# Kernel optimization log

Hardware: AMD Instinct MI355X
Metric: run time of the kernel (lower is better)

Reference implementation:

```python
import jax, jax.numpy as jnp
import numpy as np
from jax import lax

B, C, H, W = 16, 8, 512, 512
HW = H * W
AX = int(np.floor(0.1 * HW))  # torch: int(np.floor(0.1 * H * W))
EPS = 1e-5


def roberts_kernels():
    # Two 2x2 Roberts cross kernels, OIHW layout [2,1,2,2]
    kx = np.array([[1.0, 0.0], [0.0, -1.0]], np.float32)
    ky = np.array([[0.0, 1.0], [-1.0, 0.0]], np.float32)
    return jnp.asarray(np.stack([kx, ky])[:, None])


def edge_maps(x, kernels):
    # x: [N,1,H,W] -> gradient magnitude flattened to [N, HW]
    g = lax.conv_general_dilated(
        x, kernels, window_strides=(1, 1), padding=[(0, 1), (0, 1)],
        dimension_numbers=("NCHW", "OIHW", "NCHW"))  # [N,2,H,W]
    mag = jnp.sqrt(g[:, 0] ** 2 + g[:, 1] ** 2 + 1e-12)
    return mag.reshape(x.shape[0], -1)


def setup_inputs() -> dict:
    key = jax.random.key(0)
    k1, k2 = jax.random.split(key)
    return {
        "predictions": jax.random.normal(k1, (B, C, H, W), jnp.float32),
        "target": jax.random.normal(k2, (B, C, H, W), jnp.float32),
        "alpha": jnp.ones((), jnp.float32),
        "kernels": roberts_kernels(),
    }


def _forward(predictions, target, alpha, kernels):
    N = B * C
    et_all = edge_maps(target.reshape(N, 1, H, W), kernels)       # [N,HW]
    ep_all = edge_maps(predictions.reshape(N, 1, H, W), kernels)  # [N,HW]

    # Faithful to the original: edge_T_final/edge_P_final persist across
    # the (i,j) loop, so the scatter state is carried sequentially.
    def step(carry, xs):
        etf, epf = carry
        et_i, ep_i = xs
        _, tb = lax.top_k(et_i, AX)
        etf = etf.at[tb].set(et_i[tb])
        _, pb = lax.top_k(ep_i, AX)
        epf = epf.at[pb].set(ep_i[pb])
        row = jnp.abs((etf - epf) / (etf + epf + EPS))
        return (etf, epf), row

    init = (jnp.zeros(HW, jnp.float32), jnp.zeros(HW, jnp.float32))
    _, edge = lax.scan(step, init, (et_all, ep_all))  # edge: [N,HW]
    return alpha * jnp.mean(edge)


def reference(predictions, target, alpha, kernels):
    return _forward(predictions, target, alpha, kernels)
```

## Files before the change

### kernel.cpp

```cpp
#include <hip/hip_runtime.h>
#include <stdint.h>

#define H 512
#define W 512
#define HW (H * W)
#define NIMG 128
#define AX 26214
#define NB 8192
#define CAND_CAP 7168

__device__ __forceinline__ float4 f4zero() { return make_float4(0.f, 0.f, 0.f, 0.f); }

__device__ __forceinline__ void block_select(uint32_t* hist, uint32_t* chunkSuf,
                                             uint32_t* outBin, uint32_t* outRank,
                                             uint32_t K) {
  int tid = threadIdx.x;
  if (tid < 512) {
    int base = tid * 16;
    uint32_t csum = 0;
#pragma unroll
    for (int k = 0; k < 16; k++) csum += hist[base + k];
    chunkSuf[tid] = csum;
  }
  __syncthreads();
  if (tid < 64) {
    uint32_t cs[8];
    uint32_t g = 0;
#pragma unroll
    for (int m = 0; m < 8; m++) { cs[m] = chunkSuf[tid * 8 + m]; g += cs[m]; }
    uint32_t v = g;
#pragma unroll
    for (int off = 1; off < 64; off <<= 1) {
      uint32_t u = __shfl_down(v, off);
      if (tid + off < 64) v += u;
    }
    uint32_t run = v - g;
    for (int m = 7; m >= 0; m--) {
      chunkSuf[tid * 8 + m] = run;
      run += cs[m];
    }
  }
  __syncthreads();
  if (tid < 512) {
    int base = tid * 16;
    uint32_t run = chunkSuf[tid];
    for (int k = 15; k >= 0; k--) {
      uint32_t h = hist[base + k];
      if (run < K && run + h >= K) {
        *outBin = (uint32_t)(base + k);
        *outRank = K - run;
      }
      run += h;
    }
  }
  __syncthreads();
}

template <int PASS>
__device__ __forceinline__ void select_pass(const float* __restrict__ x,
                                            uint32_t* hist, uint32_t* cand,
                                            uint32_t* sCnt, uint32_t b0) {
  int tid = threadIdx.x;
  int wl = tid & 63;
  int lane_c = (tid & 127) << 2;
  int r0 = (tid >> 7) << 6;
  const bool haveE = lane_c + 4 < W;

  float4 vA, vB, vC, vD;
  float eA = 0.f, eB = 0.f, eC = 0.f, eD = 0.f;
#define LDROW(r, v, e)                                        \
  {                                                           \
    if ((r) < H) {                                            \
      v = *(const float4*)(x + (r) * W + lane_c);             \
      if (wl == 63) e = haveE ? x[(r) * W + lane_c + 4] : 0.f;\
    } else { v = f4zero(); e = 0.f; }                         \
  }
  LDROW(r0, vA, eA)
  LDROW(r0 + 1, vB, eB)
  LDROW(r0 + 2, vC, eC)
  for (int it = 0; it < 64; ++it) {
    int r = r0 + it;
    if (it < 62) { LDROW(r + 3, vD, eD) } else { vD = f4zero(); eD = 0.f; }
    float ea = __shfl(vA.x, wl + 1); if (wl == 63) ea = eA;
    float eb = __shfl(vB.x, wl + 1); if (wl == 63) eb = eB;
    float a[5] = {vA.x, vA.y, vA.z, vA.w, ea};
    float bb[5] = {vB.x, vB.y, vB.z, vB.w, eb};
#pragma unroll
    for (int j = 0; j < 4; j++) {
      float g0 = a[j] - bb[j + 1];
      float g1 = a[j + 1] - bb[j];
      float msq = fmaf(g0, g0, fmaf(g1, g1, 1e-12f));
      uint32_t bits = __float_as_uint(msq);
      if (PASS == 0) {
        atomicAdd(&hist[bits >> 19], 1u);
      } else {
        if ((bits >> 19) == b0) {
          uint32_t idx = atomicAdd(sCnt, 1u);
          if (idx < CAND_CAP) cand[idx] = bits;
        }
      }
    }
    vA = vB; eA = eB; vB = vC; eB = eC; vC = vD; eC = eD;
  }
#undef LDROW
}

__global__ __launch_bounds__(1024) void selectKernel(const float* __restrict__ target,
                                                     const float* __restrict__ pred,
                                                     float* __restrict__ thr) {
  __shared__ uint32_t hist[NB];
  __shared__ uint32_t cand[CAND_CAP];
  __shared__ uint32_t chunkSuf[512];
  __shared__ uint32_t sBin, sRank, sCnt;
  int tid = threadIdx.x;
  int b = blockIdx.x;
  int img = b & 127;
  const float* __restrict__ x = ((b >> 7) ? pred : target) + (size_t)img * HW;

  for (int i = tid; i < NB; i += 1024) hist[i] = 0;
  if (tid == 0) { sBin = 0; sRank = 1; sCnt = 0; }
  __syncthreads();

  select_pass<0>(x, hist, cand, &sCnt, 0);
  __syncthreads();
  block_select(hist, chunkSuf, &sBin, &sRank, AX);
  uint32_t b0 = sBin;
  uint32_t K1 = sRank;
  __syncthreads();

  select_pass<1>(x, hist, cand, &sCnt, b0);
  __syncthreads();
  uint32_t cnt = sCnt;
  if (cnt > CAND_CAP) cnt = CAND_CAP;

  for (int i = tid; i < NB; i += 1024) hist[i] = 0;
  __syncthreads();
  for (uint32_t j = tid; j < cnt; j += 1024)
    atomicAdd(&hist[(cand[j] >> 6) & 0x1FFFu], 1u);
  __syncthreads();
  block_select(hist, chunkSuf, &sBin, &sRank, K1);
  uint32_t b1 = sBin;
  uint32_t K2 = sRank;
  __syncthreads();

  for (int i = tid; i < NB; i += 1024) hist[i] = 0;
  __syncthreads();
  for (uint32_t j = tid; j < cnt; j += 1024) {
    uint32_t bits = cand[j];
    if (((bits >> 6) & 0x1FFFu) == b1) atomicAdd(&hist[bits & 63u], 1u);
  }
  __syncthreads();
  block_select(hist, chunkSuf, &sBin, &sRank, K2);
  if (tid == 0) {
    uint32_t tb = (b0 << 19) | (b1 << 6) | sBin;
    thr[b] = __uint_as_float(tb);
  }
}

__global__ __launch_bounds__(512, 4) void scanKernel(const float* __restrict__ target,
                                                     const float* __restrict__ pred,
                                                     const float* __restrict__ thr,
                                                     double* __restrict__ sum) {
  __shared__ float sT[NIMG], sP[NIMG];
  __shared__ float ws8[8];
  int tid = threadIdx.x;
  if (tid < NIMG) { sT[tid] = thr[tid]; sP[tid] = thr[NIMG + tid]; }
  __syncthreads();
  int b = blockIdx.x;
  int r = ((b & 7) << 6) + (b >> 3);
  int c = tid;
  int wl = tid & 63;
  const bool haveB = r + 1 < H;
  const bool edgeL = (wl == 63);
  const bool haveE = c + 1 < W;
  size_t offA = (size_t)r * W + c;
  size_t offB = offA + W;

  float tA[2], tB[2], pA[2], pB[2];
  float eT[2], eU[2], eP[2], eQ[2];

#define LOADI(i, buf)                                             \
  {                                                               \
    const float* xt = target + (size_t)(i) * HW;                  \
    const float* xp = pred + (size_t)(i) * HW;                    \
    tA[buf] = xt[offA];                                           \
    pA[buf] = xp[offA];                                           \
    tB[buf] = haveB ? xt[offB] : 0.f;                             \
    pB[buf] = haveB ? xp[offB] : 0.f;                             \
    eT[buf] = 0.f; eU[buf] = 0.f; eP[buf] = 0.f; eQ[buf] = 0.f;   \
    if (edgeL) {                                                  \
      eT[buf] = haveE ? xt[offA + 1] : 0.f;                       \
      eP[buf] = haveE ? xp[offA + 1] : 0.f;                       \
      eU[buf] = (haveE && haveB) ? xt[offB + 1] : 0.f;            \
      eQ[buf] = (haveE && haveB) ? xp[offB + 1] : 0.f;            \
    }                                                             \
  }

  float etf = 0.f, epf = 0.f, acc = 0.f;
  LOADI(0, 0)
#pragma unroll 2
  for (int i = 0; i < NIMG; ++i) {
    int cb = i & 1;
    if (i + 1 < NIMG) LOADI(i + 1, cb ^ 1)
    float tsqT = sT[i], tsqP = sP[i];
    float a1 = __shfl(tA[cb], wl + 1); if (edgeL) a1 = eT[cb];
    float b1 = __shfl(tB[cb], wl + 1); if (edgeL) b1 = eU[cb];
    float p1 = __shfl(pA[cb], wl + 1); if (edgeL) p1 = eP[cb];
    float q1 = __shfl(pB[cb], wl + 1); if (edgeL) q1 = eQ[cb];
    float g0 = tA[cb] - b1;
    float g1 = a1 - tB[cb];
    float msq = fmaf(g0, g0, fmaf(g1, g1, 1e-12f));
    if (msq >= tsqT) etf = sqrtf(msq);
    g0 = pA[cb] - q1;
    g1 = p1 - pB[cb];
    float msp = fmaf(g0, g0, fmaf(g1, g1, 1e-12f));
    if (msp >= tsqP) epf = sqrtf(msp);
    acc += fabsf((etf - epf) / (etf + epf + 1e-5f));
  }
#undef LOADI

  for (int off = 32; off; off >>= 1) acc += __shfl_down(acc, off);
  if (wl == 0) ws8[tid >> 6] = acc;
  __syncthreads();
  if (tid == 0) {
    double s = 0.0;
#pragma unroll
    for (int k = 0; k < 8; k++) s += (double)ws8[k];
    atomicAdd(sum, s);
  }
}

__global__ void initKernel(double* __restrict__ sum) { *sum = 0.0; }

__global__ void finalKernel(const double* __restrict__ sum,
                            const float* __restrict__ alpha,
                            float* __restrict__ out) {
  out[0] = (float)((double)alpha[0] * (sum[0] / (double)((double)NIMG * (double)HW)));
}

extern "C" void kernel_launch(void* const* d_in, const int* in_sizes, int n_in,
                              void* d_out, int out_size, void* d_ws, size_t ws_size,
                              hipStream_t stream) {
  const float* pred = (const float*)d_in[0];
  const float* target = (const float*)d_in[1];
  const float* alpha = (const float*)d_in[2];

  double* d_sum = (double*)d_ws;
  float* d_thr = (float*)((char*)d_ws + 64);

  initKernel<<<1, 1, 0, stream>>>(d_sum);
  selectKernel<<<256, 1024, 0, stream>>>(target, pred, d_thr);
  scanKernel<<<512, 512, 0, stream>>>(target, pred, d_thr, d_sum);
  finalKernel<<<1, 1, 0, stream>>>(d_sum, alpha, (float*)d_out);
}
```

Measured before the change: 486.9 us.

## Use sampled histogram to bracket top-k bin and fuse candidate collection into one pass

The select kernel now first builds a coarse histogram from a 1/8 row sample, picks a bin range around the expected k-th value, then makes one full pass that both builds the full histogram and collects candidates in that range. A fallback second full pass runs when the true bin falls outside the range or the candidate buffer overflows. The intent is to replace two full image passes with one in the common case, at the cost of a larger dynamic shared-memory candidate buffer. The scan kernel also replaces cross-lane shuffles with direct neighbour loads.

Measured after the change: 408.6 us. -16.1%, faster.

```diff
diff --git a/kernel.cpp b/kernel.cpp
--- a/kernel.cpp
+++ b/kernel.cpp
@@ -7,13 +7,17 @@
 #define NIMG 128
 #define AX 26214
 #define NB 8192
-#define CAND_CAP 7168
+#define CAP 12288
+#define KS 3277
+#define KM 240
+#define SMEM_WORDS (NB + CAP + 512 + 4)
+#define SMEM_BYTES (SMEM_WORDS * 4)
 
 __device__ __forceinline__ float4 f4zero() { return make_float4(0.f, 0.f, 0.f, 0.f); }
 
 __device__ __forceinline__ void block_select(uint32_t* hist, uint32_t* chunkSuf,
-                                             uint32_t* outBin, uint32_t* outRank,
-                                             uint32_t K) {
+                                             volatile uint32_t* outBin,
+                                             volatile uint32_t* outRank, uint32_t K) {
   int tid = threadIdx.x;
   if (tid < 512) {
     int base = tid * 16;
@@ -56,103 +60,160 @@
   __syncthreads();
 }
 
-template <int PASS>
-__device__ __forceinline__ void select_pass(const float* __restrict__ x,
-                                            uint32_t* hist, uint32_t* cand,
-                                            uint32_t* sCnt, uint32_t b0) {
-  int tid = threadIdx.x;
-  int wl = tid & 63;
+__device__ __forceinline__ void sample_pass(const float* __restrict__ x,
+                                            uint32_t* hist) {
+  int tid = threadIdx.x;
   int lane_c = (tid & 127) << 2;
   int r0 = (tid >> 7) << 6;
   const bool haveE = lane_c + 4 < W;
+  const float* xc = x + lane_c;
+  float4 uA[2], uB[2];
+  float fA[2], fB[2];
+#define LDS2(k, buf)                                      \
+  {                                                       \
+    const float* rp = xc + (size_t)(r0 + 8 * (k)) * W;    \
+    uA[buf] = *(const float4*)rp;                         \
+    fA[buf] = haveE ? rp[4] : 0.f;                        \
+    uB[buf] = *(const float4*)(rp + W);                   \
+    fB[buf] = haveE ? rp[W + 4] : 0.f;                    \
+  }
+  LDS2(0, 0)
+  for (int k = 0; k < 8; ++k) {
+    int cb = k & 1;
+    if (k < 7) LDS2(k + 1, cb ^ 1)
+    float a[5] = {uA[cb].x, uA[cb].y, uA[cb].z, uA[cb].w, fA[cb]};
+    float c[5] = {uB[cb].x, uB[cb].y, uB[cb].z, uB[cb].w, fB[cb]};
+#pragma unroll
+    for (int j = 0; j < 4; j++) {
+      float g0 = a[j] - c[j + 1];
+      float g1 = a[j + 1] - c[j];
+      float msq = fmaf(g0, g0, fmaf(g1, g1, 1e-12f));
+      atomicAdd(&hist[__float_as_uint(msq) >> 19], 1u);
+    }
+  }
+#undef LDS2
+}
+
+template <int HIST>
+__device__ __forceinline__ void full_pass(const float* __restrict__ x,
+                                          uint32_t* hist, uint32_t* cand,
+                                          uint32_t* sCnt, uint32_t lo,
+                                          uint32_t span) {
+  int tid = threadIdx.x;
+  int lane_c = (tid & 127) << 2;
+  int r0 = (tid >> 7) << 6;
+  const bool haveE = lane_c + 4 < W;
+  const float* xc = x + lane_c;
 
   float4 vA, vB, vC, vD;
   float eA = 0.f, eB = 0.f, eC = 0.f, eD = 0.f;
-#define LDROW(r, v, e)                                        \
-  {                                                           \
-    if ((r) < H) {                                            \
-      v = *(const float4*)(x + (r) * W + lane_c);             \
-      if (wl == 63) e = haveE ? x[(r) * W + lane_c + 4] : 0.f;\
-    } else { v = f4zero(); e = 0.f; }                         \
-  }
-  LDROW(r0, vA, eA)
-  LDROW(r0 + 1, vB, eB)
-  LDROW(r0 + 2, vC, eC)
+#define LDR(r, v, e)                                  \
+  {                                                   \
+    if ((r) < H) {                                    \
+      const float* rp = xc + (size_t)(r) * W;         \
+      v = *(const float4*)rp;                         \
+      e = haveE ? rp[4] : 0.f;                        \
+    } else { v = f4zero(); e = 0.f; }                 \
+  }
+  LDR(r0, vA, eA)
+  LDR(r0 + 1, vB, eB)
+  LDR(r0 + 2, vC, eC)
   for (int it = 0; it < 64; ++it) {
     int r = r0 + it;
-    if (it < 62) { LDROW(r + 3, vD, eD) } else { vD = f4zero(); eD = 0.f; }
-    float ea = __shfl(vA.x, wl + 1); if (wl == 63) ea = eA;
-    float eb = __shfl(vB.x, wl + 1); if (wl == 63) eb = eB;
-    float a[5] = {vA.x, vA.y, vA.z, vA.w, ea};
-    float bb[5] = {vB.x, vB.y, vB.z, vB.w, eb};
+    if (it < 62) { LDR(r + 3, vD, eD) } else { vD = f4zero(); eD = 0.f; }
+    float a[5] = {vA.x, vA.y, vA.z, vA.w, eA};
+    float c[5] = {vB.x, vB.y, vB.z, vB.w, eB};
 #pragma unroll
     for (int j = 0; j < 4; j++) {
-      float g0 = a[j] - bb[j + 1];
-      float g1 = a[j + 1] - bb[j];
+      float g0 = a[j] - c[j + 1];
+      float g1 = a[j + 1] - c[j];
       float msq = fmaf(g0, g0, fmaf(g1, g1, 1e-12f));
       uint32_t bits = __float_as_uint(msq);
-      if (PASS == 0) {
-        atomicAdd(&hist[bits >> 19], 1u);
-      } else {
-        if ((bits >> 19) == b0) {
-          uint32_t idx = atomicAdd(sCnt, 1u);
-          if (idx < CAND_CAP) cand[idx] = bits;
-        }
+      uint32_t bin = bits >> 19;
+      if (HIST) atomicAdd(&hist[bin], 1u);
+      if (bin - lo <= span) {
+        uint32_t idx = atomicAdd(sCnt, 1u);
+        if (idx < CAP) cand[idx] = bits;
       }
     }
     vA = vB; eA = eB; vB = vC; eB = eC; vC = vD; eC = eD;
   }
-#undef LDROW
+#undef LDR
 }
 
 __global__ __launch_bounds__(1024) void selectKernel(const float* __restrict__ target,
                                                      const float* __restrict__ pred,
                                                      float* __restrict__ thr) {
-  __shared__ uint32_t hist[NB];
-  __shared__ uint32_t cand[CAND_CAP];
-  __shared__ uint32_t chunkSuf[512];
-  __shared__ uint32_t sBin, sRank, sCnt;
+  extern __shared__ uint32_t smem[];
+  uint32_t* hist = smem;
+  uint32_t* cand = smem + NB;
+  uint32_t* chunkSuf = smem + NB + CAP;
+  volatile uint32_t* sBin = smem + NB + CAP + 512;
+  volatile uint32_t* sRank = smem + NB + CAP + 513;
+  uint32_t* sCnt = smem + NB + CAP + 514;
+
   int tid = threadIdx.x;
   int b = blockIdx.x;
   int img = b & 127;
   const float* __restrict__ x = ((b >> 7) ? pred : target) + (size_t)img * HW;
 
   for (int i = tid; i < NB; i += 1024) hist[i] = 0;
-  if (tid == 0) { sBin = 0; sRank = 1; sCnt = 0; }
-  __syncthreads();
-
-  select_pass<0>(x, hist, cand, &sCnt, 0);
-  __syncthreads();
-  block_select(hist, chunkSuf, &sBin, &sRank, AX);
-  uint32_t b0 = sBin;
-  uint32_t K1 = sRank;
-  __syncthreads();
-
-  select_pass<1>(x, hist, cand, &sCnt, b0);
-  __syncthreads();
-  uint32_t cnt = sCnt;
-  if (cnt > CAND_CAP) cnt = CAND_CAP;
+  if (tid == 0) *sCnt = 0;
+  __syncthreads();
+
+  sample_pass(x, hist);
+  __syncthreads();
+  block_select(hist, chunkSuf, sBin, sRank, KS - KM);
+  uint32_t bHi = *sBin;
+  block_select(hist, chunkSuf, sBin, sRank, KS + KM);
+  uint32_t bLo = *sBin;
+  __syncthreads();
 
   for (int i = tid; i < NB; i += 1024) hist[i] = 0;
   __syncthreads();
-  for (uint32_t j = tid; j < cnt; j += 1024)
-    atomicAdd(&hist[(cand[j] >> 6) & 0x1FFFu], 1u);
-  __syncthreads();
-  block_select(hist, chunkSuf, &sBin, &sRank, K1);
-  uint32_t b1 = sBin;
-  uint32_t K2 = sRank;
-  __syncthreads();
+
+  full_pass<1>(x, hist, cand, sCnt, bLo, bHi - bLo);
+  __syncthreads();
+  block_select(hist, chunkSuf, sBin, sRank, AX);
+  uint32_t b0 = *sBin;
+  uint32_t K1 = *sRank;
+  uint32_t cnt = *sCnt;
+  __syncthreads();
+
+  bool bad = (b0 < bLo) || (b0 > bHi) || (cnt > CAP);
+  if (bad) {
+    if (tid == 0) *sCnt = 0;
+    __syncthreads();
+    full_pass<0>(x, hist, cand, sCnt, b0, 0);
+    __syncthreads();
+    cnt = *sCnt;
+    __syncthreads();
+  }
+  if (cnt > CAP) cnt = CAP;
 
   for (int i = tid; i < NB; i += 1024) hist[i] = 0;
   __syncthreads();
   for (uint32_t j = tid; j < cnt; j += 1024) {
     uint32_t bits = cand[j];
-    if (((bits >> 6) & 0x1FFFu) == b1) atomicAdd(&hist[bits & 63u], 1u);
-  }
-  __syncthreads();
-  block_select(hist, chunkSuf, &sBin, &sRank, K2);
+    if ((bits >> 19) == b0) atomicAdd(&hist[(bits >> 6) & 0x1FFFu], 1u);
+  }
+  __syncthreads();
+  block_select(hist, chunkSuf, sBin, sRank, K1);
+  uint32_t b1 = *sBin;
+  uint32_t K2 = *sRank;
+  __syncthreads();
+
+  for (int i = tid; i < NB; i += 1024) hist[i] = 0;
+  __syncthreads();
+  for (uint32_t j = tid; j < cnt; j += 1024) {
+    uint32_t bits = cand[j];
+    if ((bits >> 19) == b0 && ((bits >> 6) & 0x1FFFu) == b1)
+      atomicAdd(&hist[bits & 63u], 1u);
+  }
+  __syncthreads();
+  block_select(hist, chunkSuf, sBin, sRank, K2);
   if (tid == 0) {
-    uint32_t tb = (b0 << 19) | (b1 << 6) | sBin;
+    uint32_t tb = (b0 << 19) | (b1 << 6) | *sBin;
     thr[b] = __uint_as_float(tb);
   }
 }
@@ -169,31 +230,26 @@
   int b = blockIdx.x;
   int r = ((b & 7) << 6) + (b >> 3);
   int c = tid;
-  int wl = tid & 63;
   const bool haveB = r + 1 < H;
-  const bool edgeL = (wl == 63);
   const bool haveE = c + 1 < W;
   size_t offA = (size_t)r * W + c;
   size_t offB = offA + W;
 
-  float tA[2], tB[2], pA[2], pB[2];
-  float eT[2], eU[2], eP[2], eQ[2];
-
-#define LOADI(i, buf)                                             \
-  {                                                               \
-    const float* xt = target + (size_t)(i) * HW;                  \
-    const float* xp = pred + (size_t)(i) * HW;                    \
-    tA[buf] = xt[offA];                                           \
-    pA[buf] = xp[offA];                                           \
-    tB[buf] = haveB ? xt[offB] : 0.f;                             \
-    pB[buf] = haveB ? xp[offB] : 0.f;                             \
-    eT[buf] = 0.f; eU[buf] = 0.f; eP[buf] = 0.f; eQ[buf] = 0.f;   \
-    if (edgeL) {                                                  \
-      eT[buf] = haveE ? xt[offA + 1] : 0.f;                       \
-      eP[buf] = haveE ? xp[offA + 1] : 0.f;                       \
-      eU[buf] = (haveE && haveB) ? xt[offB + 1] : 0.f;            \
-      eQ[buf] = (haveE && haveB) ? xp[offB + 1] : 0.f;            \
-    }                                                             \
+  float t00[2], t01[2], t10[2], t11[2];
+  float p00[2], p01[2], p10[2], p11[2];
+
+#define LOADI(i, buf)                                         \
+  {                                                           \
+    const float* xt = target + (size_t)(i) * HW;              \
+    const float* xp = pred + (size_t)(i) * HW;                \
+    t00[buf] = xt[offA];                                      \
+    t01[buf] = haveE ? xt[offA + 1] : 0.f;                    \
+    t10[buf] = haveB ? xt[offB] : 0.f;                        \
+    t11[buf] = (haveB && haveE) ? xt[offB + 1] : 0.f;         \
+    p00[buf] = xp[offA];                                      \
+    p01[buf] = haveE ? xp[offA + 1] : 0.f;                    \
+    p10[buf] = haveB ? xp[offB] : 0.f;                        \
+    p11[buf] = (haveB && haveE) ? xp[offB + 1] : 0.f;         \
   }
 
   float etf = 0.f, epf = 0.f, acc = 0.f;
@@ -203,16 +259,12 @@
     int cb = i & 1;
     if (i + 1 < NIMG) LOADI(i + 1, cb ^ 1)
     float tsqT = sT[i], tsqP = sP[i];
-    float a1 = __shfl(tA[cb], wl + 1); if (edgeL) a1 = eT[cb];
-    float b1 = __shfl(tB[cb], wl + 1); if (edgeL) b1 = eU[cb];
-    float p1 = __shfl(pA[cb], wl + 1); if (edgeL) p1 = eP[cb];
-    float q1 = __shfl(pB[cb], wl + 1); if (edgeL) q1 = eQ[cb];
-    float g0 = tA[cb] - b1;
-    float g1 = a1 - tB[cb];
+    float g0 = t00[cb] - t11[cb];
+    float g1 = t01[cb] - t10[cb];
     float msq = fmaf(g0, g0, fmaf(g1, g1, 1e-12f));
     if (msq >= tsqT) etf = sqrtf(msq);
-    g0 = pA[cb] - q1;
-    g1 = p1 - pB[cb];
+    g0 = p00[cb] - p11[cb];
+    g1 = p01[cb] - p10[cb];
     float msp = fmaf(g0, g0, fmaf(g1, g1, 1e-12f));
     if (msp >= tsqP) epf = sqrtf(msp);
     acc += fabsf((etf - epf) / (etf + epf + 1e-5f));
@@ -220,7 +272,7 @@
 #undef LOADI
 
   for (int off = 32; off; off >>= 1) acc += __shfl_down(acc, off);
-  if (wl == 0) ws8[tid >> 6] = acc;
+  if ((tid & 63) == 0) ws8[tid >> 6] = acc;
   __syncthreads();
   if (tid == 0) {
     double s = 0.0;
@@ -248,8 +300,15 @@
   double* d_sum = (double*)d_ws;
   float* d_thr = (float*)((char*)d_ws + 64);
 
+  static int attrSet = 0;
+  if (!attrSet) {
+    hipFuncSetAttribute(reinterpret_cast<const void*>(&selectKernel),
+                        hipFuncAttributeMaxDynamicSharedMemorySize, SMEM_BYTES);
+    attrSet = 1;
+  }
+
   initKernel<<<1, 1, 0, stream>>>(d_sum);
-  selectKernel<<<256, 1024, 0, stream>>>(target, pred, d_thr);
+  selectKernel<<<256, 1024, SMEM_BYTES, stream>>>(target, pred, d_thr);
   scanKernel<<<512, 512, 0, stream>>>(target, pred, d_thr, d_sum);
   finalKernel<<<1, 1, 0, stream>>>(d_sum, alpha, (float*)d_out);
 }
```
